# Kernel tuning notes

Hardware: AMD Instinct MI355X
Metric: run time of the kernel (lower is better)

## Reference

```python
import jax, jax.numpy as jnp
import numpy as np

D_MODEL = 2048
D_STATE = 64
D_CONV = 4
EXPAND = 2
HEADDIM = 64
NGROUPS = 1
CHUNK = 64
D_INNER = D_MODEL * EXPAND          # 4096
NHEADS = D_INNER // HEADDIM         # 64
D_IN_PROJ = 2 * D_INNER + 2 * NGROUPS * D_STATE + NHEADS
BATCH, SEQLEN = 2, 4096
RMS_EPS = 1e-6


def elu_plus_one(x):
    return jax.nn.elu(x) + 1.0


def softplus(x):
    return jnp.where(x > 20, x, jnp.log1p(jnp.exp(x)))


def causal_conv1d(x, w, b):
    # x: (B, L, D), w: (K, D) depthwise kernel, b: (D,)
    Bsz, L, Dn = x.shape
    k = w.shape[0]
    xp = jnp.transpose(jnp.pad(x, ((0, 0), (k - 1, 0), (0, 0))), (0, 2, 1))  # (B, D, L+K-1)
    kern = jnp.transpose(w, (1, 0))[:, None, :]  # (D, 1, K)
    y = jax.lax.conv_general_dilated(xp, kern, (1,), 'VALID',
                                     feature_group_count=Dn,
                                     dimension_numbers=('NCH', 'OIH', 'NCH'))
    return jnp.transpose(y, (0, 2, 1)) + b


def ssd_chunked(q, k, v, a, chunk_size):
    # SSD / chunked linear attention with per-step scalar decay.
    # Recurrence: h_t = a_t * h_{t-1} + k_t v_t^T ; y_t = q_t @ h_t
    # q,k: (B,H,L,N); v: (B,H,L,P); a: (B,H,L) in (0,1)
    Bsz, H, L, N = q.shape
    S = chunk_size
    C = L // S
    qc = q.reshape(Bsz, H, C, S, N)
    kc = k.reshape(Bsz, H, C, S, N)
    vc = v.reshape(Bsz, H, C, S, -1)
    la = jnp.log(a).reshape(Bsz, H, C, S)
    cs = jnp.cumsum(la, axis=-1)                 # inclusive cumsum of log-decay within chunk
    causal = jnp.tril(jnp.ones((S, S), bool))
    # decay from position j to i (j<=i): exp(cs_i - cs_j)
    logdec = jnp.where(causal, cs[..., :, None] - cs[..., None, :], -jnp.inf)
    att = jnp.einsum('bhcsn,bhctn->bhcst', qc, kc) * jnp.exp(logdec)
    y_intra = jnp.einsum('bhcst,bhctp->bhcsp', att, vc)
    total = cs[..., -1]                           # (B,H,C) total log-decay per chunk
    k_scaled = kc * jnp.exp(total[..., None, None] - cs[..., None])
    states = jnp.einsum('bhcsn,bhcsp->bhcnp', k_scaled, vc)  # per-chunk state update
    d_t = jnp.moveaxis(jnp.exp(total), 2, 0)      # (C,B,H)
    s_t = jnp.moveaxis(states, 2, 0)              # (C,B,H,N,P)

    def step(h, inp):
        d, s = inp
        return d[..., None, None] * h + s, h      # emit state at chunk start

    _, h_prev = jax.lax.scan(step, jnp.zeros_like(s_t[0]), (d_t, s_t))
    h_prev = jnp.moveaxis(h_prev, 0, 2)           # (B,H,C,N,P)
    y_inter = jnp.einsum('bhcsn,bhcnp->bhcsp', qc * jnp.exp(cs)[..., None], h_prev)
    return (y_intra + y_inter).reshape(Bsz, H, L, -1)


def setup_inputs() -> dict:
    key = jax.random.key(0)
    k0, k1, k2, k3 = jax.random.split(key, 4)
    u = jax.random.normal(k0, (BATCH, SEQLEN, D_MODEL), jnp.float32)
    in_proj_w = jax.random.normal(k1, (D_MODEL, D_IN_PROJ), jnp.float32) / np.sqrt(D_MODEL)
    conv_weight = jax.random.normal(k2, (D_CONV, D_INNER), jnp.float32) / np.sqrt(D_CONV)
    conv_bias = jnp.zeros((D_INNER,), jnp.float32)
    A_log = jnp.log(jnp.linspace(1.0, 16.0, NHEADS)).astype(jnp.float32)
    dt_init = jnp.exp(jnp.linspace(np.log(0.001), np.log(0.1), NHEADS))
    dt_bias = (dt_init + jnp.log(-jnp.expm1(-dt_init))).astype(jnp.float32)
    D_param = jnp.ones((NHEADS,), jnp.float32)
    norm_scale = jnp.ones((D_INNER,), jnp.float32)
    out_proj_w = jax.random.normal(k3, (D_INNER, D_MODEL), jnp.float32) / np.sqrt(D_INNER)
    return dict(u=u, in_proj_w=in_proj_w, conv_weight=conv_weight, conv_bias=conv_bias,
                A_log=A_log, dt_bias=dt_bias, D_param=D_param, norm_scale=norm_scale,
                out_proj_w=out_proj_w)


def reference(u, in_proj_w, conv_weight, conv_bias, A_log, dt_bias, D_param, norm_scale, out_proj_w):
    Bsz, L, _ = u.shape
    zxBCdt = u @ in_proj_w
    splits = [D_INNER, 2 * D_INNER, 2 * D_INNER + NGROUPS * D_STATE, 2 * D_INNER + 2 * NGROUPS * D_STATE]
    z, x, B_proj, C_proj, dt_logits = jnp.split(zxBCdt, splits, axis=-1)
    x = jax.nn.silu(causal_conv1d(x, conv_weight, conv_bias))
    B_mat = elu_plus_one(B_proj.reshape(Bsz, L, NGROUPS, D_STATE))
    C_mat = elu_plus_one(C_proj.reshape(Bsz, L, NGROUPS, D_STATE))
    hpg = NHEADS // NGROUPS
    B_mat = jnp.repeat(B_mat, hpg, axis=2)   # (B,L,H,N)
    C_mat = jnp.repeat(C_mat, hpg, axis=2)
    dt = softplus(dt_logits + dt_bias)        # (B,L,H)
    a = jnp.exp(-dt * jnp.exp(A_log))         # (B,L,H), per-step decay
    x_heads = x.reshape(Bsz, L, NHEADS, HEADDIM)
    q = jnp.transpose(C_mat, (0, 2, 1, 3))
    k = jnp.transpose(B_mat, (0, 2, 1, 3))
    v = jnp.transpose(x_heads, (0, 2, 1, 3))
    a_t = jnp.transpose(a, (0, 2, 1))
    y = ssd_chunked(q, k, v, a_t, CHUNK)
    y = y + D_param[None, :, None, None] * v  # skip connection
    y = jnp.transpose(y, (0, 2, 1, 3)).reshape(Bsz, L, D_INNER)
    y = y * jax.lax.rsqrt(jnp.mean(y * y, axis=-1, keepdims=True) + RMS_EPS) * norm_scale
    y = y * jax.nn.silu(z)
    return y @ out_proj_w
```

## Files before the change

kernel.cpp:

```cpp
#include <hip/hip_runtime.h>
#include <hip/hip_bf16.h>
#include <cstdint>
#include <cstddef>

#define BATCH   2
#define SEQLEN  4096
#define DMODEL  2048
#define DINNER  4096
#define NHEADS  64
#define HEADDIM 64
#define DSTATE  64
#define CHUNK   64
#define NCHUNK  (SEQLEN/CHUNK)
#define DPROJ   8384
#define DPROJ_PAD 8448
#define MTOK    (BATCH*SEQLEN)
#define RMS_EPS 1e-6f

typedef __hip_bfloat16 bf16;
typedef __attribute__((ext_vector_type(8))) short bf16x8;
typedef __attribute__((ext_vector_type(4))) float f32x4;

__device__ __forceinline__ float siluf(float x) { return x / (1.f + expf(-x)); }
__device__ __forceinline__ float to_f(float x) { return x; }
__device__ __forceinline__ float to_f(bf16 x) { return __bfloat162float(x); }
__device__ __forceinline__ float bf2f(short s) { bf16 h; *(short*)&h = s; return __bfloat162float(h); }
__device__ __forceinline__ void from_f(float& d, float x) { d = x; }
__device__ __forceinline__ void from_f(bf16& d, float x) { d = __float2bfloat16(x); }

__device__ __forceinline__ void gload16(const void* g, void* l) {
  __builtin_amdgcn_global_load_lds(
      (const __attribute__((address_space(1))) void*)g,
      (__attribute__((address_space(3))) void*)l, 16, 0, 0);
}

template <typename TC, bool MASK, int KT>
__global__ __launch_bounds__(512, 2) void gemm_u(
    const bf16* __restrict__ A, int lda,
    const bf16* __restrict__ BT, int ldb,
    TC* __restrict__ C, int ldc, int Nvalid, int gx) {
  __shared__ __align__(16) bf16 As[4 * 8192];
  __shared__ __align__(16) bf16 Bs[4 * 8192];
  const int tid  = threadIdx.x;
  const int lane = tid & 63;
  const int w    = tid >> 6;
  const int wm   = w >> 2;
  const int wn   = w & 3;
  const int lr   = lane & 15, lg = lane >> 4;
  const int fo   = 8 * (lg ^ ((lr >> 1) & 3));

  int nwg = gridDim.x;
  int bid = (int)blockIdx.x;
  int idx = (bid & 7) * (nwg >> 3) + (bid >> 3);
  int spos = idx % (8 * gx);
  const int m0 = ((idx / (8 * gx)) * 8 + (spos & 7)) * 256;
  const int n0 = (spos >> 3) * 256;

  const int srow = tid >> 2;
  const int ce   = 8 * ((tid & 3) ^ ((tid >> 3) & 3));
  const bf16* pA0 = A  + (size_t)(m0 + srow)       * lda + ce;
  const bf16* pA1 = A  + (size_t)(m0 + 128 + srow) * lda + ce;
  const bf16* pB0 = BT + (size_t)(n0 + srow)       * ldb + ce;
  const bf16* pB1 = BT + (size_t)(n0 + 128 + srow) * ldb + ce;
  const int wofs = w * 512;
  const int aRd = (wm * 128 + lr) * 32 + fo;
  const int bRd = (wn * 64 + lr) * 32 + fo;

#define STAGE_A(kt) do {                                       \
    bf16* d_ = As + (((kt) & 3) << 13);  int kk_ = (kt) << 5;  \
    gload16(pA0 + kk_, d_ + wofs);                             \
    gload16(pA1 + kk_, d_ + 4096 + wofs);                      \
  } while (0)
#define STAGE_B(kt) do {                                       \
    bf16* d_ = Bs + (((kt) & 3) << 13);  int kk_ = (kt) << 5;  \
    gload16(pB0 + kk_, d_ + wofs);                             \
    gload16(pB1 + kk_, d_ + 4096 + wofs);                      \
  } while (0)

  f32x4 acc[8][4];
#pragma unroll
  for (int m = 0; m < 8; ++m)
#pragma unroll
    for (int n = 0; n < 4; ++n) acc[m][n] = (f32x4){0.f, 0.f, 0.f, 0.f};

#define KBODY(T, DOSTAGE, VMC) do {                                          \
    const bf16* Ab = As + (((T) & 3) << 13);                                 \
    const bf16* Bb = Bs + (((T) & 3) << 13);                                 \
    if (DOSTAGE) { STAGE_A((T) + 3); STAGE_B((T) + 3); }                     \
    bf16x8 bfv[4], af[4], ag[4];                                             \
    _Pragma("unroll")                                                        \
    for (int n = 0; n < 4; ++n) bfv[n] = *(const bf16x8*)&Bb[bRd + n * 512]; \
    _Pragma("unroll")                                                        \
    for (int m = 0; m < 4; ++m) af[m] = *(const bf16x8*)&Ab[aRd + m * 512];  \
    __builtin_amdgcn_sched_barrier(0);                                       \
    _Pragma("unroll")                                                        \
    for (int m = 0; m < 4; ++m) ag[m] = *(const bf16x8*)&Ab[aRd + (m + 4) * 512]; \
    asm volatile("s_waitcnt lgkmcnt(4)" ::: "memory");                       \
    __builtin_amdgcn_sched_barrier(0);                                       \
    __builtin_amdgcn_s_setprio(1);                                           \
    _Pragma("unroll")                                                        \
    for (int m = 0; m < 4; ++m)                                              \
      _Pragma("unroll")                                                      \
      for (int n = 0; n < 4; ++n)                                            \
        acc[m][n] = __builtin_amdgcn_mfma_f32_16x16x32_bf16(af[m], bfv[n], acc[m][n], 0, 0, 0); \
    asm volatile("s_waitcnt lgkmcnt(0)" ::: "memory");                       \
    __builtin_amdgcn_sched_barrier(0);                                       \
    _Pragma("unroll")                                                        \
    for (int m = 0; m < 4; ++m)                                              \
      _Pragma("unroll")                                                      \
      for (int n = 0; n < 4; ++n)                                            \
        acc[m + 4][n] = __builtin_amdgcn_mfma_f32_16x16x32_bf16(ag[m], bfv[n], acc[m + 4][n], 0, 0, 0); \
    __builtin_amdgcn_s_setprio(0);                                           \
    asm volatile("s_waitcnt vmcnt(" #VMC ")" ::: "memory");                  \
    __builtin_amdgcn_s_barrier();                                            \
    __builtin_amdgcn_sched_barrier(0);                                       \
  } while (0)

  STAGE_A(0); STAGE_B(0); STAGE_A(1); STAGE_B(1); STAGE_A(2); STAGE_B(2);
  asm volatile("s_waitcnt vmcnt(8)" ::: "memory");
  __builtin_amdgcn_s_barrier();
  __builtin_amdgcn_sched_barrier(0);

#pragma unroll 4
  for (int t = 0; t < KT - 3; ++t) KBODY(t, true, 8);
  KBODY(KT - 3, false, 4);
  KBODY(KT - 2, false, 0);
  KBODY(KT - 1, false, 0);
#undef KBODY
#undef STAGE_A
#undef STAGE_B

  if constexpr (__is_same(TC, bf16)) {
    bf16* Ws = (w < 4 ? As : Bs) + (w & 3) * 8192;
#pragma unroll
    for (int m = 0; m < 8; ++m)
#pragma unroll
      for (int n = 0; n < 4; ++n)
#pragma unroll
        for (int reg = 0; reg < 4; ++reg) {
          int row = m * 16 + lg * 4 + reg;
          int slot = (n * 2 + (lr >> 3)) ^ (row & 7);
          Ws[row * 64 + slot * 8 + (lr & 7)] = __float2bfloat16(acc[m][n][reg]);
        }
    asm volatile("s_waitcnt lgkmcnt(0)" ::: "memory");
#pragma unroll
    for (int i = 0; i < 16; ++i) {
      int row = i * 8 + (lane >> 3);
      bf16x8 v = *(const bf16x8*)&Ws[row * 64 + ((lane & 7) ^ (lane >> 3)) * 8];
      int gcol = n0 + wn * 64 + (lane & 7) * 8;
      if (!MASK || gcol < Nvalid)
        *(bf16x8*)&((bf16*)C)[(size_t)(m0 + wm * 128 + row) * ldc + gcol] = v;
    }
  } else {
#pragma unroll
    for (int m = 0; m < 8; ++m)
#pragma unroll
      for (int n = 0; n < 4; ++n) {
        int col = n0 + wn * 64 + n * 16 + lr;
        if (MASK && col >= Nvalid) continue;
        size_t rbase = (size_t)(m0 + wm * 128 + m * 16 + lg * 4);
#pragma unroll
        for (int reg = 0; reg < 4; ++reg)
          from_f(C[(rbase + reg) * ldc + col], acc[m][n][reg]);
      }
  }
}

__global__ __launch_bounds__(256) void cast_bf16_kernel(
    const float* __restrict__ x, bf16* __restrict__ y) {
  size_t i = ((size_t)blockIdx.x * 256 + threadIdx.x) * 4;
  float4 v = *(const float4*)(x + i);
  y[i + 0] = __float2bfloat16(v.x);
  y[i + 1] = __float2bfloat16(v.y);
  y[i + 2] = __float2bfloat16(v.z);
  y[i + 3] = __float2bfloat16(v.w);
}

__global__ __launch_bounds__(256) void transpose_cast_kernel(
    const float* __restrict__ W, bf16* __restrict__ WT, int N, int K) {
  __shared__ float t[32][33];
  int n0 = blockIdx.x * 32, k0 = blockIdx.y * 32;
  int tx = threadIdx.x & 31, ty = threadIdx.x >> 5;
#pragma unroll
  for (int i = 0; i < 4; ++i) {
    int n = n0 + tx;
    t[ty + i * 8][tx] = (n < N) ? W[(size_t)(k0 + ty + i * 8) * N + n] : 0.f;
  }
  __syncthreads();
#pragma unroll
  for (int i = 0; i < 4; ++i) {
    int nn = ty + i * 8;
    WT[(size_t)(n0 + nn) * K + k0 + tx] = __float2bfloat16(t[tx][nn]);
  }
}

__global__ __launch_bounds__(256) void conv_silu_kernel(
    const bf16* __restrict__ zx, const float* __restrict__ cw,
    const float* __restrict__ cb, bf16* __restrict__ xc) {
  int idx = blockIdx.x * 256 + threadIdx.x;
  int d8 = (idx & 511) * 8;
  int m = idx >> 9;
  int l = m & (SEQLEN - 1);
  int b = m >> 12;
  float acc[8];
#pragma unroll
  for (int j = 0; j < 8; ++j) acc[j] = cb[d8 + j];
#pragma unroll
  for (int k = 0; k < 4; ++k) {
    int li = l - 3 + k;
    if (li >= 0) {
      bf16x8 xv = *(const bf16x8*)&zx[(size_t)(b * SEQLEN + li) * DPROJ + DINNER + d8];
      const float* cwp = cw + k * DINNER + d8;
#pragma unroll
      for (int j = 0; j < 8; ++j) acc[j] += bf2f(xv[j]) * cwp[j];
    }
  }
  bf16x8 o;
#pragma unroll
  for (int j = 0; j < 8; ++j) { bf16 h = __float2bfloat16(siluf(acc[j])); o[j] = *(short*)&h; }
  *(bf16x8*)&xc[(size_t)m * DINNER + d8] = o;
}

__global__ __launch_bounds__(256) void prep_kernel(
    const bf16* __restrict__ zx, const float* __restrict__ A_log,
    const float* __restrict__ dt_bias, bf16* __restrict__ Bmb,
    bf16* __restrict__ Cmb, float* __restrict__ la) {
  int idx = blockIdx.x * 256 + threadIdx.x;
  int j = idx & 63;
  int m = idx >> 6;
  const bf16* row = zx + (size_t)m * DPROJ;
  float bv = to_f(row[2 * DINNER + j]);
  float cv = to_f(row[2 * DINNER + DSTATE + j]);
  float dtl = to_f(row[2 * DINNER + 2 * DSTATE + j]) + dt_bias[j];
  from_f(Bmb[idx], bv > 0.f ? bv + 1.f : expf(bv));
  from_f(Cmb[idx], cv > 0.f ? cv + 1.f : expf(cv));
  float dt = dtl > 20.f ? dtl : log1pf(expf(dtl));
  la[idx] = -dt * expf(A_log[j]);
}

__global__ __launch_bounds__(64) void cumsum_kernel(
    const float* __restrict__ la, float* __restrict__ cs) {
  int bid = blockIdx.x;
  int c = bid & 63, h = (bid >> 6) & 63, b = bid >> 12;
  int s = threadIdx.x;
  __shared__ float lds[64];
  size_t base = (size_t)(b * SEQLEN + c * CHUNK + s) * 64 + h;
  lds[s] = la[base];
  __syncthreads();
  float acc = 0.f;
  for (int t = 0; t <= s; ++t) acc += lds[t];
  cs[base] = acc;
}

__global__ __launch_bounds__(256) void states_mfma(
    const bf16* __restrict__ Bmb, const bf16* __restrict__ xc,
    const float* __restrict__ cs, bf16* __restrict__ st) {
  int bid = blockIdx.x;
  int c = bid & 63, h = (bid >> 6) & 63, b = bid >> 12;
  int m0 = b * SEQLEN + c * CHUNK;
  int tid = threadIdx.x, lane = tid & 63, w = tid >> 6;
  int lr = lane & 15, lg = lane >> 4;
  __shared__ bf16 vT[64 * 72];
  __shared__ bf16 kT[64 * 72];
  int s4 = tid >> 2, c16 = (tid & 3) * 16;
  float cstot = cs[(size_t)(m0 + 63) * 64 + h];
  float ws = expf(cstot - cs[(size_t)(m0 + s4) * 64 + h]);
  {
    union { bf16x8 v[2]; bf16 hh[16]; } u;
    const bf16x8* pv = (const bf16x8*)&xc[(size_t)(m0 + s4) * DINNER + h * 64 + c16];
    u.v[0] = pv[0]; u.v[1] = pv[1];
#pragma unroll
    for (int i = 0; i < 16; ++i) vT[(c16 + i) * 72 + s4] = u.hh[i];
    const bf16x8* pk = (const bf16x8*)&Bmb[(size_t)(m0 + s4) * 64 + c16];
    u.v[0] = pk[0]; u.v[1] = pk[1];
#pragma unroll
    for (int i = 0; i < 16; ++i) kT[(c16 + i) * 72 + s4] = __float2bfloat16(to_f(u.hh[i]) * ws);
  }
  __syncthreads();
  f32x4 acc[4];
#pragma unroll
  for (int ct = 0; ct < 4; ++ct) acc[ct] = (f32x4){0.f, 0.f, 0.f, 0.f};
#pragma unroll
  for (int ks = 0; ks < 2; ++ks) {
    bf16x8 af = *(const bf16x8*)&vT[(w * 16 + lr) * 72 + ks * 32 + lg * 8];
#pragma unroll
    for (int ct = 0; ct < 4; ++ct) {
      bf16x8 bf_ = *(const bf16x8*)&kT[(ct * 16 + lr) * 72 + ks * 32 + lg * 8];
      acc[ct] = __builtin_amdgcn_mfma_f32_16x16x32_bf16(af, bf_, acc[ct], 0, 0, 0);
    }
  }
  size_t ob = (((size_t)(b * NHEADS + h)) * NCHUNK + c) * 4096;
#pragma unroll
  for (int ct = 0; ct < 4; ++ct) {
    int n = ct * 16 + lr;
#pragma unroll
    for (int r = 0; r < 4; ++r) {
      int p = w * 16 + lg * 4 + r;
      from_f(st[ob + (size_t)p * 64 + n], acc[ct][r]);
    }
  }
}

__global__ __launch_bounds__(256) void scan_kernel(
    const float* __restrict__ cs, bf16* __restrict__ st) {
  int bid = blockIdx.x;
  int bh = bid >> 2, qq = bid & 3;
  int b = bh >> 6, h = bh & 63;
  int e0 = qq * 1024 + threadIdx.x * 4;
  float hr[4] = {0.f, 0.f, 0.f, 0.f};
  size_t base = (size_t)bh * NCHUNK * 4096;
  typedef __attribute__((ext_vector_type(4))) short bf16x4;
  for (int c = 0; c < NCHUNK; ++c) {
    float d = expf(cs[(size_t)(b * SEQLEN + c * CHUNK + 63) * 64 + h]);
    bf16* p = st + base + (size_t)c * 4096 + e0;
    union { bf16x4 v; bf16 hh[4]; } in, out;
    in.v = *(bf16x4*)p;
#pragma unroll
    for (int i = 0; i < 4; ++i) {
      float sv = to_f(in.hh[i]);
      from_f(out.hh[i], hr[i]);
      hr[i] = d * hr[i] + sv;
    }
    *(bf16x4*)p = out.v;
  }
}

__global__ __launch_bounds__(256) void chunk_out_mfma(
    const bf16* __restrict__ Bmb, const bf16* __restrict__ Cmb,
    const bf16* __restrict__ xc, const float* __restrict__ cs,
    const bf16* __restrict__ st, const float* __restrict__ Dp,
    bf16* __restrict__ zx) {
  int bid = blockIdx.x;
  int c = bid & 63, h = (bid >> 6) & 63, b = bid >> 12;
  int m0 = b * SEQLEN + c * CHUNK;
  int tid = threadIdx.x, lane = tid & 63, w = tid >> 6;
  int lr = lane & 15, lg = lane >> 4;
  __shared__ bf16 qL[64 * 72];
  __shared__ bf16 kL[64 * 72];
  __shared__ bf16 A2[64 * 136];
  __shared__ bf16 B2[64 * 136];
  __shared__ float csl[64];
  int s4 = tid >> 2, c16 = (tid & 3) * 16;

  if (tid < 64) csl[tid] = cs[(size_t)(m0 + tid) * 64 + h];
  {
    const bf16x8* pq = (const bf16x8*)&Cmb[(size_t)(m0 + s4) * 64 + c16];
    *(bf16x8*)&qL[s4 * 72 + c16] = pq[0];
    *(bf16x8*)&qL[s4 * 72 + c16 + 8] = pq[1];
    const bf16x8* pk = (const bf16x8*)&Bmb[(size_t)(m0 + s4) * 64 + c16];
    *(bf16x8*)&kL[s4 * 72 + c16] = pk[0];
    *(bf16x8*)&kL[s4 * 72 + c16 + 8] = pk[1];
  }
  {
    union { bf16x8 v[2]; bf16 hh[16]; } u;
    const bf16x8* pv = (const bf16x8*)&xc[(size_t)(m0 + s4) * DINNER + h * 64 + c16];
    u.v[0] = pv[0]; u.v[1] = pv[1];
#pragma unroll
    for (int i = 0; i < 16; ++i) B2[(c16 + i) * 136 + s4] = u.hh[i];
  }
  {
    size_t hb = (((size_t)(b * NHEADS + h)) * NCHUNK + c) * 4096;
    const bf16x8* ph = (const bf16x8*)&st[hb + (size_t)s4 * 64 + c16];
    *(bf16x8*)&B2[s4 * 136 + 64 + c16] = ph[0];
    *(bf16x8*)&B2[s4 * 136 + 64 + c16 + 8] = ph[1];
  }
  __syncthreads();

  f32x4 acc1[4];
#pragma unroll
  for (int ct = 0; ct < 4; ++ct) acc1[ct] = (f32x4){0.f, 0.f, 0.f, 0.f};
#pragma unroll
  for (int ks = 0; ks < 2; ++ks) {
    bf16x8 af = *(const bf16x8*)&qL[(w * 16 + lr) * 72 + ks * 32 + lg * 8];
#pragma unroll
    for (int ct = 0; ct < 4; ++ct) {
      bf16x8 bf_ = *(const bf16x8*)&kL[(ct * 16 + lr) * 72 + ks * 32 + lg * 8];
      acc1[ct] = __builtin_amdgcn_mfma_f32_16x16x32_bf16(af, bf_, acc1[ct], 0, 0, 0);
    }
  }
  {
    float es = expf(csl[s4]);
    union { bf16x8 v[2]; bf16 hh[16]; } u;
    const bf16x8* pq = (const bf16x8*)&qL[s4 * 72 + c16];
    u.v[0] = pq[0]; u.v[1] = pq[1];
#pragma unroll
    for (int i = 0; i < 16; ++i) u.hh[i] = __float2bfloat16(to_f(u.hh[i]) * es);
    *(bf16x8*)&A2[s4 * 136 + 64 + c16] = u.v[0];
    *(bf16x8*)&A2[s4 * 136 + 64 + c16 + 8] = u.v[1];
  }
#pragma unroll
  for (int ct = 0; ct < 4; ++ct) {
    int t = ct * 16 + lr;
#pragma unroll
    for (int r = 0; r < 4; ++r) {
      int s = w * 16 + lg * 4 + r;
      float val = (t <= s) ? acc1[ct][r] * expf(csl[s] - csl[t]) : 0.f;
      A2[s * 136 + t] = __float2bfloat16(val);
    }
  }
  __syncthreads();

  float Dh = Dp[h];
  f32x4 acc2[4];
#pragma unroll
  for (int ct = 0; ct < 4; ++ct) {
    int p = ct * 16 + lr;
#pragma unroll
    for (int r = 0; r < 4; ++r)
      acc2[ct][r] = Dh * to_f(B2[p * 136 + (w * 16 + lg * 4 + r)]);
  }
#pragma unroll
  for (int ks = 0; ks < 4; ++ks) {
    bf16x8 af = *(const bf16x8*)&A2[(w * 16 + lr) * 136 + ks * 32 + lg * 8];
#pragma unroll
    for (int ct = 0; ct < 4; ++ct) {
      bf16x8 bf_ = *(const bf16x8*)&B2[(ct * 16 + lr) * 136 + ks * 32 + lg * 8];
      acc2[ct] = __builtin_amdgcn_mfma_f32_16x16x32_bf16(af, bf_, acc2[ct], 0, 0, 0);
    }
  }
  __syncthreads();
#pragma unroll
  for (int ct = 0; ct < 4; ++ct) {
    int p = ct * 16 + lr;
#pragma unroll
    for (int r = 0; r < 4; ++r)
      qL[(w * 16 + lg * 4 + r) * 72 + p] = __float2bfloat16(acc2[ct][r]);
  }
  __syncthreads();
  {
    const bf16x8* py = (const bf16x8*)&qL[s4 * 72 + c16];
    bf16x8* pg = (bf16x8*)&zx[(size_t)(m0 + s4) * DPROJ + DINNER + h * 64 + c16];
    pg[0] = py[0]; pg[1] = py[1];
  }
}

__global__ __launch_bounds__(256) void rmsnorm_gate_kernel(
    bf16* __restrict__ zx, const float* __restrict__ scale) {
  int m = blockIdx.x;
  int tid = threadIdx.x;
  bf16* row = zx + (size_t)m * DPROJ;
  float vals[16];
  float ss = 0.f;
#pragma unroll
  for (int g = 0; g < 2; ++g) {
    int d8 = (tid + g * 256) * 8;
    bf16x8 yv = *(const bf16x8*)&row[DINNER + d8];
#pragma unroll
    for (int j = 0; j < 8; ++j) {
      float y = bf2f(yv[j]);
      vals[g * 8 + j] = y;
      ss += y * y;
    }
  }
#pragma unroll
  for (int off = 32; off > 0; off >>= 1) ss += __shfl_down(ss, off, 64);
  __shared__ float red[4];
  if ((tid & 63) == 0) red[tid >> 6] = ss;
  __syncthreads();
  float tot = red[0] + red[1] + red[2] + red[3];
  float inv = rsqrtf(tot / (float)DINNER + RMS_EPS);
#pragma unroll
  for (int g = 0; g < 2; ++g) {
    int d8 = (tid + g * 256) * 8;
    bf16x8 zv = *(const bf16x8*)&row[d8];
    const float* sc = scale + d8;
    bf16x8 o;
#pragma unroll
    for (int j = 0; j < 8; ++j) {
      bf16 hh = __float2bfloat16(vals[g * 8 + j] * inv * sc[j] * siluf(bf2f(zv[j])));
      o[j] = *(short*)&hh;
    }
    *(bf16x8*)&row[DINNER + d8] = o;
  }
}

extern "C" void kernel_launch(void* const* d_in, const int* in_sizes, int n_in,
                              void* d_out, int out_size, void* d_ws, size_t ws_size,
                              hipStream_t stream) {
  const float* u       = (const float*)d_in[0];
  const float* Win     = (const float*)d_in[1];
  const float* cw      = (const float*)d_in[2];
  const float* cb      = (const float*)d_in[3];
  const float* A_log   = (const float*)d_in[4];
  const float* dt_bias = (const float*)d_in[5];
  const float* Dp      = (const float*)d_in[6];
  const float* nscale  = (const float*)d_in[7];
  const float* Wout    = (const float*)d_in[8];
  float* out = (float*)d_out;

  bf16* zx = (bf16*)d_ws;
  bf16* xc = zx + (size_t)MTOK * DPROJ;
  bf16* ub = xc;
  bf16* wT = xc + (size_t)MTOK * DINNER;
  bf16* Bmb = wT + (size_t)DPROJ_PAD * DMODEL;
  bf16* Cmb = Bmb + (size_t)MTOK * 64;
  float* la = (float*)(Cmb + (size_t)MTOK * 64);
  float* cs = la + (size_t)MTOK * 64;
  bf16* st = (bf16*)d_out;

  cast_bf16_kernel<<<(MTOK * DMODEL) / (256 * 4), 256, 0, stream>>>(u, ub);
  transpose_cast_kernel<<<dim3(DPROJ_PAD / 32, DMODEL / 32), 256, 0, stream>>>(Win, wT, DPROJ, DMODEL);
  gemm_u<bf16, true, DMODEL / 32><<<(DPROJ_PAD / 256) * (MTOK / 256), 512, 0, stream>>>(
      ub, DMODEL, wT, DMODEL, zx, DPROJ, DPROJ, DPROJ_PAD / 256);
  transpose_cast_kernel<<<dim3(DMODEL / 32, DINNER / 32), 256, 0, stream>>>(Wout, wT, DMODEL, DINNER);
  conv_silu_kernel<<<(MTOK * 512) / 256, 256, 0, stream>>>(zx, cw, cb, xc);
  prep_kernel<<<(MTOK * 64) / 256, 256, 0, stream>>>(zx, A_log, dt_bias, Bmb, Cmb, la);
  cumsum_kernel<<<BATCH * NHEADS * NCHUNK, 64, 0, stream>>>(la, cs);
  states_mfma<<<BATCH * NHEADS * NCHUNK, 256, 0, stream>>>(Bmb, xc, cs, st);
  scan_kernel<<<BATCH * NHEADS * 4, 256, 0, stream>>>(cs, st);
  chunk_out_mfma<<<BATCH * NHEADS * NCHUNK, 256, 0, stream>>>(Bmb, Cmb, xc, cs, st, Dp, zx);
  rmsnorm_gate_kernel<<<MTOK, 256, 0, stream>>>(zx, nscale);
  gemm_u<float, false, DINNER / 32><<<(DMODEL / 256) * (MTOK / 256), 512, 0, stream>>>(
      zx + DINNER, DPROJ, wT, DINNER, out, DMODEL, DMODEL, DMODEL / 256);
}
```

Measured before the change: 665.7 us.

## Restructure GEMM into 8-phase double-buffered K64 pipeline and prefetch scan loads

The GEMM is rewritten from a 4-stage K=32 ring into two K=64 LDS slots with an 8-phase schedule. Global-to-LDS loads are interleaved between MFMA phases, with a new XOR swizzle and barriers in every phase. The aim is to hide load latency better and cut barrier overhead per unit of K for both projection GEMMs. The scan kernel also prefetches chunk states three iterations ahead so global loads overlap the serial recurrence. The trade-off is more barriers per iteration and a subtle, easily broken staging order.

```diff
diff --git a/kernel.cpp b/kernel.cpp
--- a/kernel.cpp
+++ b/kernel.cpp
@@ -34,20 +34,21 @@
       (__attribute__((address_space(3))) void*)l, 16, 0, 0);
 }
 
-template <typename TC, bool MASK, int KT>
-__global__ __launch_bounds__(512, 2) void gemm_u(
+#define WAITV(n) asm volatile("s_waitcnt vmcnt(" #n ")" ::: "memory")
+
+template <typename TC, bool MASK, int NI>
+__global__ __launch_bounds__(512, 2) void gemm_8p(
     const bf16* __restrict__ A, int lda,
     const bf16* __restrict__ BT, int ldb,
     TC* __restrict__ C, int ldc, int Nvalid, int gx) {
-  __shared__ __align__(16) bf16 As[4 * 8192];
-  __shared__ __align__(16) bf16 Bs[4 * 8192];
+  __shared__ __align__(16) bf16 As[2 * 16384];
+  __shared__ __align__(16) bf16 Bs[2 * 16384];
   const int tid  = threadIdx.x;
   const int lane = tid & 63;
   const int w    = tid >> 6;
   const int wm   = w >> 2;
   const int wn   = w & 3;
   const int lr   = lane & 15, lg = lane >> 4;
-  const int fo   = 8 * (lg ^ ((lr >> 1) & 3));
 
   int nwg = gridDim.x;
   int bid = (int)blockIdx.x;
@@ -56,25 +57,24 @@
   const int m0 = ((idx / (8 * gx)) * 8 + (spos & 7)) * 256;
   const int n0 = (spos >> 3) * 256;
 
-  const int srow = tid >> 2;
-  const int ce   = 8 * ((tid & 3) ^ ((tid >> 3) & 3));
-  const bf16* pA0 = A  + (size_t)(m0 + srow)       * lda + ce;
-  const bf16* pA1 = A  + (size_t)(m0 + 128 + srow) * lda + ce;
-  const bf16* pB0 = BT + (size_t)(n0 + srow)       * ldb + ce;
-  const bf16* pB1 = BT + (size_t)(n0 + 128 + srow) * ldb + ce;
-  const int wofs = w * 512;
-  const int aRd = (wm * 128 + lr) * 32 + fo;
-  const int bRd = (wn * 64 + lr) * 32 + fo;
-
-#define STAGE_A(kt) do {                                       \
-    bf16* d_ = As + (((kt) & 3) << 13);  int kk_ = (kt) << 5;  \
-    gload16(pA0 + kk_, d_ + wofs);                             \
-    gload16(pA1 + kk_, d_ + 4096 + wofs);                      \
+  const int srow8 = tid >> 3;
+  const int ce    = 8 * ((tid & 7) ^ ((tid >> 3) & 7));
+  const bf16* gA = A  + (size_t)(m0 + srow8) * lda + ce;
+  const bf16* gB = BT + (size_t)(n0 + srow8) * ldb + ce;
+  const int dofs = w * 512;
+
+  const int abase = (wm * 128 + lr) * 64;
+  const int bbase = (wn * 64 + lr) * 64;
+  const int col0 = ((0 + lg) ^ (lr & 7)) * 8;
+  const int col1 = ((4 + lg) ^ (lr & 7)) * 8;
+
+#define ST_A(SL, kt, R0) do { \
+    gload16(gA + (size_t)(R0) * lda + (kt) * 64,        As + (SL) * 16384 + ((R0) + 0) * 64 + dofs);  \
+    gload16(gA + (size_t)((R0) + 64) * lda + (kt) * 64, As + (SL) * 16384 + ((R0) + 64) * 64 + dofs); \
   } while (0)
-#define STAGE_B(kt) do {                                       \
-    bf16* d_ = Bs + (((kt) & 3) << 13);  int kk_ = (kt) << 5;  \
-    gload16(pB0 + kk_, d_ + wofs);                             \
-    gload16(pB1 + kk_, d_ + 4096 + wofs);                      \
+#define ST_B(SL, kt, R0) do { \
+    gload16(gB + (size_t)(R0) * ldb + (kt) * 64,        Bs + (SL) * 16384 + ((R0) + 0) * 64 + dofs);  \
+    gload16(gB + (size_t)((R0) + 64) * ldb + (kt) * 64, Bs + (SL) * 16384 + ((R0) + 64) * 64 + dofs); \
   } while (0)
 
   f32x4 acc[8][4];
@@ -82,53 +82,68 @@
   for (int m = 0; m < 8; ++m)
 #pragma unroll
     for (int n = 0; n < 4; ++n) acc[m][n] = (f32x4){0.f, 0.f, 0.f, 0.f};
-
-#define KBODY(T, DOSTAGE, VMC) do {                                          \
-    const bf16* Ab = As + (((T) & 3) << 13);                                 \
-    const bf16* Bb = Bs + (((T) & 3) << 13);                                 \
-    if (DOSTAGE) { STAGE_A((T) + 3); STAGE_B((T) + 3); }                     \
-    bf16x8 bfv[4], af[4], ag[4];                                             \
-    _Pragma("unroll")                                                        \
-    for (int n = 0; n < 4; ++n) bfv[n] = *(const bf16x8*)&Bb[bRd + n * 512]; \
-    _Pragma("unroll")                                                        \
-    for (int m = 0; m < 4; ++m) af[m] = *(const bf16x8*)&Ab[aRd + m * 512];  \
-    __builtin_amdgcn_sched_barrier(0);                                       \
-    _Pragma("unroll")                                                        \
-    for (int m = 0; m < 4; ++m) ag[m] = *(const bf16x8*)&Ab[aRd + (m + 4) * 512]; \
-    asm volatile("s_waitcnt lgkmcnt(4)" ::: "memory");                       \
-    __builtin_amdgcn_sched_barrier(0);                                       \
-    __builtin_amdgcn_s_setprio(1);                                           \
-    _Pragma("unroll")                                                        \
-    for (int m = 0; m < 4; ++m)                                              \
-      _Pragma("unroll")                                                      \
-      for (int n = 0; n < 4; ++n)                                            \
-        acc[m][n] = __builtin_amdgcn_mfma_f32_16x16x32_bf16(af[m], bfv[n], acc[m][n], 0, 0, 0); \
-    asm volatile("s_waitcnt lgkmcnt(0)" ::: "memory");                       \
-    __builtin_amdgcn_sched_barrier(0);                                       \
-    _Pragma("unroll")                                                        \
-    for (int m = 0; m < 4; ++m)                                              \
-      _Pragma("unroll")                                                      \
-      for (int n = 0; n < 4; ++n)                                            \
-        acc[m + 4][n] = __builtin_amdgcn_mfma_f32_16x16x32_bf16(ag[m], bfv[n], acc[m + 4][n], 0, 0, 0); \
-    __builtin_amdgcn_s_setprio(0);                                           \
-    asm volatile("s_waitcnt vmcnt(" #VMC ")" ::: "memory");                  \
-    __builtin_amdgcn_s_barrier();                                            \
-    __builtin_amdgcn_sched_barrier(0);                                       \
+  bf16x8 bq[4][2];
+
+#define PHASE(SL, Q, RDB, STCODE, VMC) do {                                   \
+    if (RDB) {                                                                \
+      _Pragma("unroll")                                                       \
+      for (int nf = 0; nf < 4; ++nf) {                                        \
+        bq[nf][0] = *(const bf16x8*)&Bs[(SL) * 16384 + bbase + nf * 1024 + col0]; \
+        bq[nf][1] = *(const bf16x8*)&Bs[(SL) * 16384 + bbase + nf * 1024 + col1]; \
+      }                                                                       \
+    }                                                                         \
+    bf16x8 a00 = *(const bf16x8*)&As[(SL) * 16384 + abase + (2 * (Q)) * 1024 + col0];     \
+    bf16x8 a01 = *(const bf16x8*)&As[(SL) * 16384 + abase + (2 * (Q)) * 1024 + col1];     \
+    bf16x8 a10 = *(const bf16x8*)&As[(SL) * 16384 + abase + (2 * (Q) + 1) * 1024 + col0]; \
+    bf16x8 a11 = *(const bf16x8*)&As[(SL) * 16384 + abase + (2 * (Q) + 1) * 1024 + col1]; \
+    STCODE;                                                                   \
+    __builtin_amdgcn_s_barrier();                                             \
+    asm volatile("s_waitcnt lgkmcnt(0)" ::: "memory");                        \
+    __builtin_amdgcn_sched_barrier(0);                                        \
+    __builtin_amdgcn_s_setprio(1);                                            \
+    _Pragma("unroll")                                                         \
+    for (int nf = 0; nf < 4; ++nf)                                            \
+      acc[2 * (Q)][nf] = __builtin_amdgcn_mfma_f32_16x16x32_bf16(a00, bq[nf][0], acc[2 * (Q)][nf], 0, 0, 0); \
+    _Pragma("unroll")                                                         \
+    for (int nf = 0; nf < 4; ++nf)                                            \
+      acc[2 * (Q) + 1][nf] = __builtin_amdgcn_mfma_f32_16x16x32_bf16(a10, bq[nf][0], acc[2 * (Q) + 1][nf], 0, 0, 0); \
+    _Pragma("unroll")                                                         \
+    for (int nf = 0; nf < 4; ++nf)                                            \
+      acc[2 * (Q)][nf] = __builtin_amdgcn_mfma_f32_16x16x32_bf16(a01, bq[nf][1], acc[2 * (Q)][nf], 0, 0, 0); \
+    _Pragma("unroll")                                                         \
+    for (int nf = 0; nf < 4; ++nf)                                            \
+      acc[2 * (Q) + 1][nf] = __builtin_amdgcn_mfma_f32_16x16x32_bf16(a11, bq[nf][1], acc[2 * (Q) + 1][nf], 0, 0, 0); \
+    __builtin_amdgcn_s_setprio(0);                                            \
+    VMC;                                                                      \
+    __builtin_amdgcn_s_barrier();                                             \
+    __builtin_amdgcn_sched_barrier(0);                                        \
   } while (0)
 
-  STAGE_A(0); STAGE_B(0); STAGE_A(1); STAGE_B(1); STAGE_A(2); STAGE_B(2);
-  asm volatile("s_waitcnt vmcnt(8)" ::: "memory");
+#define ITER(IT, LAST) do {                                                   \
+    PHASE(0, 0, true,  { ST_A(1, 2 * (IT) + 1, 0); ST_A(1, 2 * (IT) + 1, 128); }, ;); \
+    PHASE(0, 1, false, { if (!(LAST)) ST_B(0, 2 * (IT) + 2, 0); }, ;);        \
+    PHASE(0, 2, false, { if (!(LAST)) ST_B(0, 2 * (IT) + 2, 128); }, ;);      \
+    PHASE(0, 3, false, { ; }, { if (LAST) { WAITV(0); } else { WAITV(4); } });\
+    PHASE(1, 0, true,  { if (!(LAST)) ST_A(0, 2 * (IT) + 2, 0); }, ;);        \
+    PHASE(1, 1, false, { if (!(LAST)) ST_A(0, 2 * (IT) + 2, 128); }, ;);      \
+    PHASE(1, 2, false, { if (!(LAST)) ST_B(1, 2 * (IT) + 3, 0); }, ;);        \
+    PHASE(1, 3, false, { ; }, { if (LAST) { WAITV(0); } else { ST_B(1, 2 * (IT) + 3, 128); WAITV(4); } }); \
+  } while (0)
+
+  ST_B(0, 0, 0); ST_B(0, 0, 128);
+  ST_A(0, 0, 0); ST_A(0, 0, 128);
+  ST_B(1, 1, 0); ST_B(1, 1, 128);
+  WAITV(4);
   __builtin_amdgcn_s_barrier();
   __builtin_amdgcn_sched_barrier(0);
 
-#pragma unroll 4
-  for (int t = 0; t < KT - 3; ++t) KBODY(t, true, 8);
-  KBODY(KT - 3, false, 4);
-  KBODY(KT - 2, false, 0);
-  KBODY(KT - 1, false, 0);
-#undef KBODY
-#undef STAGE_A
-#undef STAGE_B
+#pragma unroll 2
+  for (int it = 0; it < NI - 1; ++it) ITER(it, false);
+  ITER(NI - 1, true);
+#undef ITER
+#undef PHASE
+#undef ST_A
+#undef ST_B
 
   if constexpr (__is_same(TC, bf16)) {
     bf16* Ws = (w < 4 ? As : Bs) + (w & 3) * 8192;
@@ -310,18 +325,24 @@
   float hr[4] = {0.f, 0.f, 0.f, 0.f};
   size_t base = (size_t)bh * NCHUNK * 4096;
   typedef __attribute__((ext_vector_type(4))) short bf16x4;
+  union U { bf16x4 v; bf16 hh[4]; };
+  U buf[4];
+  buf[0].v = *(bf16x4*)(st + base + 0 * 4096 + e0);
+  buf[1].v = *(bf16x4*)(st + base + 1 * 4096 + e0);
+  buf[2].v = *(bf16x4*)(st + base + 2 * 4096 + e0);
+#pragma unroll 4
   for (int c = 0; c < NCHUNK; ++c) {
+    if (c + 3 < NCHUNK)
+      buf[(c + 3) & 3].v = *(bf16x4*)(st + base + (size_t)(c + 3) * 4096 + e0);
     float d = expf(cs[(size_t)(b * SEQLEN + c * CHUNK + 63) * 64 + h]);
-    bf16* p = st + base + (size_t)c * 4096 + e0;
-    union { bf16x4 v; bf16 hh[4]; } in, out;
-    in.v = *(bf16x4*)p;
+    U out;
 #pragma unroll
     for (int i = 0; i < 4; ++i) {
-      float sv = to_f(in.hh[i]);
+      float sv = to_f(buf[c & 3].hh[i]);
       from_f(out.hh[i], hr[i]);
       hr[i] = d * hr[i] + sv;
     }
-    *(bf16x4*)p = out.v;
+    *(bf16x4*)(st + base + (size_t)c * 4096 + e0) = out.v;
   }
 }
 
@@ -500,7 +521,7 @@
 
   cast_bf16_kernel<<<(MTOK * DMODEL) / (256 * 4), 256, 0, stream>>>(u, ub);
   transpose_cast_kernel<<<dim3(DPROJ_PAD / 32, DMODEL / 32), 256, 0, stream>>>(Win, wT, DPROJ, DMODEL);
-  gemm_u<bf16, true, DMODEL / 32><<<(DPROJ_PAD / 256) * (MTOK / 256), 512, 0, stream>>>(
+  gemm_8p<bf16, true, DMODEL / 128><<<(DPROJ_PAD / 256) * (MTOK / 256), 512, 0, stream>>>(
       ub, DMODEL, wT, DMODEL, zx, DPROJ, DPROJ, DPROJ_PAD / 256);
   transpose_cast_kernel<<<dim3(DMODEL / 32, DINNER / 32), 256, 0, stream>>>(Wout, wT, DMODEL, DINNER);
   conv_silu_kernel<<<(MTOK * 512) / 256, 256, 0, stream>>>(zx, cw, cb, xc);
@@ -510,6 +531,6 @@
   scan_kernel<<<BATCH * NHEADS * 4, 256, 0, stream>>>(cs, st);
   chunk_out_mfma<<<BATCH * NHEADS * NCHUNK, 256, 0, stream>>>(Bmb, Cmb, xc, cs, st, Dp, zx);
   rmsnorm_gate_kernel<<<MTOK, 256, 0, stream>>>(zx, nscale);
-  gemm_u<float, false, DINNER / 32><<<(DMODEL / 256) * (MTOK / 256), 512, 0, stream>>>(
+  gemm_8p<float, false, DINNER / 128><<<(DMODEL / 256) * (MTOK / 256), 512, 0, stream>>>(
       zx + DINNER, DPROJ, wT, DINNER, out, DMODEL, DMODEL, DMODEL / 256);
 }
```

Result: no change. 674.4 us (+1.3%).

## Split in-projection GEMM tail to a smaller-tile kernel and prefetch scan loads

Applied to the files above, without the earlier changes.

The input-projection GEMM now runs its 256-wide tile kernel only over the first 2*DINNER columns, which divide evenly. A new 128x128 MFMA kernel handles the remaining 192 columns (B, C, dt), so the old padded tail tile is no longer computed at full 256 width. The scan kernel precomputes the per-chunk decays into shared memory and software-pipelines the state loads three chunks ahead, hiding global latency in its serial loop. The cost is an extra kernel launch, and the small tail GEMM grid (2 x 64 blocks) may underuse the device.

```diff
diff --git a/kernel.cpp b/kernel.cpp
--- a/kernel.cpp
+++ b/kernel.cpp
@@ -166,6 +166,74 @@
   }
 }
 
+template <typename TC, bool MASK>
+__global__ __launch_bounds__(256) void gemm_mfma(
+    const bf16* __restrict__ A, int lda,
+    const bf16* __restrict__ BT, int ldb,
+    TC* __restrict__ C, int ldc, int Kdim, int Nvalid) {
+  __shared__ __align__(16) bf16 As[128 * 32];
+  __shared__ __align__(16) bf16 Bs[128 * 32];
+  const int tid  = threadIdx.x;
+  const int lane = tid & 63;
+  const int w    = tid >> 6;
+  const int m0 = blockIdx.y * 128;
+  const int n0 = blockIdx.x * 128;
+
+  const int rs0 = w * 32 + (lane >> 2);
+  const int ce  = 8 * ((lane & 3) ^ ((lane >> 2) & 3));
+  const int fo  = 8 * ((lane >> 4) ^ (lane & 3));
+  const int lr  = lane & 15, lg = lane >> 4;
+  const int wr = w >> 1, wc = w & 1;
+
+  f32x4 acc[4][4];
+#pragma unroll
+  for (int m = 0; m < 4; ++m)
+#pragma unroll
+    for (int n = 0; n < 4; ++n) acc[m][n] = (f32x4){0.f, 0.f, 0.f, 0.f};
+
+  const size_t arow0 = (size_t)(m0 + rs0) * lda;
+  const size_t arow1 = (size_t)(m0 + rs0 + 16) * lda;
+  const size_t brow0 = (size_t)(n0 + rs0) * ldb;
+  const size_t brow1 = (size_t)(n0 + rs0 + 16) * ldb;
+  bf16* lA0 = &As[(w * 2 + 0) * 512];
+  bf16* lA1 = &As[(w * 2 + 1) * 512];
+  bf16* lB0 = &Bs[(w * 2 + 0) * 512];
+  bf16* lB1 = &Bs[(w * 2 + 1) * 512];
+
+  for (int k0 = 0; k0 < Kdim; k0 += 32) {
+    __syncthreads();
+    gload16(A + arow0 + k0 + ce, lA0);
+    gload16(A + arow1 + k0 + ce, lA1);
+    gload16(BT + brow0 + k0 + ce, lB0);
+    gload16(BT + brow1 + k0 + ce, lB1);
+    __syncthreads();
+    bf16x8 af[4], bfr[4];
+#pragma unroll
+    for (int m = 0; m < 4; ++m)
+      af[m] = *(const bf16x8*)&As[(wr * 64 + m * 16 + lr) * 32 + fo];
+#pragma unroll
+    for (int n = 0; n < 4; ++n)
+      bfr[n] = *(const bf16x8*)&Bs[(wc * 64 + n * 16 + lr) * 32 + fo];
+#pragma unroll
+    for (int m = 0; m < 4; ++m)
+#pragma unroll
+      for (int n = 0; n < 4; ++n)
+        acc[m][n] = __builtin_amdgcn_mfma_f32_16x16x32_bf16(af[m], bfr[n], acc[m][n], 0, 0, 0);
+  }
+
+#pragma unroll
+  for (int m = 0; m < 4; ++m)
+#pragma unroll
+    for (int n = 0; n < 4; ++n) {
+      int col = n0 + wc * 64 + n * 16 + lr;
+      if (MASK && col >= Nvalid) continue;
+      size_t rbase = (size_t)(m0 + wr * 64 + m * 16 + lg * 4);
+#pragma unroll
+      for (int reg = 0; reg < 4; ++reg)
+        from_f(C[(rbase + reg) * ldc + col], acc[m][n][reg]);
+    }
+}
+
 __global__ __launch_bounds__(256) void cast_bf16_kernel(
     const float* __restrict__ x, bf16* __restrict__ y) {
   size_t i = ((size_t)blockIdx.x * 256 + threadIdx.x) * 4;
@@ -306,22 +374,33 @@
   int bid = blockIdx.x;
   int bh = bid >> 2, qq = bid & 3;
   int b = bh >> 6, h = bh & 63;
-  int e0 = qq * 1024 + threadIdx.x * 4;
+  int tid = threadIdx.x;
+  __shared__ float dec[64];
+  if (tid < 64)
+    dec[tid] = expf(cs[(size_t)(b * SEQLEN + tid * CHUNK + 63) * 64 + h]);
+  int e0 = qq * 1024 + tid * 4;
   float hr[4] = {0.f, 0.f, 0.f, 0.f};
   size_t base = (size_t)bh * NCHUNK * 4096;
   typedef __attribute__((ext_vector_type(4))) short bf16x4;
+  union U { bf16x4 v; bf16 hh[4]; };
+  U buf[4];
+  buf[0].v = *(bf16x4*)(st + base + 0 * 4096 + e0);
+  buf[1].v = *(bf16x4*)(st + base + 1 * 4096 + e0);
+  buf[2].v = *(bf16x4*)(st + base + 2 * 4096 + e0);
+  __syncthreads();
+#pragma unroll 4
   for (int c = 0; c < NCHUNK; ++c) {
-    float d = expf(cs[(size_t)(b * SEQLEN + c * CHUNK + 63) * 64 + h]);
-    bf16* p = st + base + (size_t)c * 4096 + e0;
-    union { bf16x4 v; bf16 hh[4]; } in, out;
-    in.v = *(bf16x4*)p;
+    if (c + 3 < NCHUNK)
+      buf[(c + 3) & 3].v = *(bf16x4*)(st + base + (size_t)(c + 3) * 4096 + e0);
+    float d = dec[c];
+    U out;
 #pragma unroll
     for (int i = 0; i < 4; ++i) {
-      float sv = to_f(in.hh[i]);
+      float sv = to_f(buf[c & 3].hh[i]);
       from_f(out.hh[i], hr[i]);
       hr[i] = d * hr[i] + sv;
     }
-    *(bf16x4*)p = out.v;
+    *(bf16x4*)(st + base + (size_t)c * 4096 + e0) = out.v;
   }
 }
 
@@ -500,8 +579,11 @@
 
   cast_bf16_kernel<<<(MTOK * DMODEL) / (256 * 4), 256, 0, stream>>>(u, ub);
   transpose_cast_kernel<<<dim3(DPROJ_PAD / 32, DMODEL / 32), 256, 0, stream>>>(Win, wT, DPROJ, DMODEL);
-  gemm_u<bf16, true, DMODEL / 32><<<(DPROJ_PAD / 256) * (MTOK / 256), 512, 0, stream>>>(
-      ub, DMODEL, wT, DMODEL, zx, DPROJ, DPROJ, DPROJ_PAD / 256);
+  gemm_u<bf16, false, DMODEL / 32><<<(2 * DINNER / 256) * (MTOK / 256), 512, 0, stream>>>(
+      ub, DMODEL, wT, DMODEL, zx, DPROJ, DPROJ, 2 * DINNER / 256);
+  gemm_mfma<bf16, true><<<dim3(2, MTOK / 128), 256, 0, stream>>>(
+      ub, DMODEL, wT + (size_t)(2 * DINNER) * DMODEL, DMODEL,
+      zx + 2 * DINNER, DPROJ, DMODEL, 2 * DINNER + 192 - (2 * DINNER));
   transpose_cast_kernel<<<dim3(DMODEL / 32, DINNER / 32), 256, 0, stream>>>(Wout, wT, DMODEL, DINNER);
   conv_silu_kernel<<<(MTOK * 512) / 256, 256, 0, stream>>>(zx, cw, cb, xc);
   prep_kernel<<<(MTOK * 64) / 256, 256, 0, stream>>>(zx, A_log, dt_bias, Bmb, Cmb, la);
```

After: 662.6 us. About the same (-0.5%).
